# Optimization experiments

Measured on AMD Instinct MI355X. Metric: run time of the kernel, lower is better.

## Reference

```python
import math
import jax, jax.numpy as jnp
import numpy as np

N_EXPERTS = 8
CAPACITY_FACTOR = 1.25
AUX_COEF = 0.01  # forward passes aux_loss_coef to BOTH z-loss and lb-loss


def setup_inputs() -> dict:
    key = jax.random.key(0)
    k1, k2 = jax.random.split(key)
    B, T, D = 4, 4096, 2048
    x = jax.random.normal(k1, (B, T, D), dtype=jnp.float32)
    # nn.Linear(d_model, n_experts, bias=False) weight: (n_experts, d_model)
    W = jax.random.normal(k2, (N_EXPERTS, D), dtype=jnp.float32) * (1.0 / math.sqrt(D))
    return {"x": x, "W": W}


def reference(x, W):
    B, T, D = x.shape
    S = B * T
    E = W.shape[0]
    capacity = int(math.ceil(S / E * CAPACITY_FACTOR))  # static

    x_flat = x.reshape(S, D)
    logits = jnp.einsum("sd,ed->se", x_flat, W)          # (S, E)
    probs = jax.nn.softmax(logits, axis=-1)               # (S, E)
    gate_vals = jnp.max(probs, axis=-1)                   # (S,)
    expert_idx = jnp.argmax(probs, axis=-1)               # (S,) int

    # rank of each token within its expert's queue (token order), 0-based
    onehot = jax.nn.one_hot(expert_idx, E, dtype=jnp.int32)        # (S, E)
    rank = jnp.sum(jnp.cumsum(onehot, axis=0) * onehot, axis=-1) - 1  # (S,)
    keep = rank < capacity
    kept_gates = jnp.where(keep, gate_vals, jnp.zeros((), gate_vals.dtype))

    # z-loss: coef * mean(logsumexp(logits)^2)
    log_z = jax.scipy.special.logsumexp(logits, axis=-1)
    z_loss = AUX_COEF * jnp.mean(log_z * log_z)

    # load-balance loss: coef * E * sum(f_i * p_i)
    p = jnp.mean(probs, axis=0)                                     # (E,)
    counts = jnp.zeros((E,), dtype=probs.dtype).at[expert_idx].add(1.0)
    f = counts / S
    lb_loss = AUX_COEF * E * jnp.sum(f * p)

    aux_loss = z_loss + lb_loss
    return expert_idx, kept_gates, aux_loss
```

## Files before the change

kernel.cpp:

```cpp
#include <hip/hip_runtime.h>

#define S_TOKENS 16384
#define DMODEL   2048
#define NE       8
#define CAPACITY 2560
#define AUXC     0.01f


__global__ void init_kernel(float* __restrict__ acc) {
    int t = threadIdx.x;
    if (t < 9) acc[t] = 0.0f;
}

__global__ __launch_bounds__(512, 1) void logits_kernel(
    const float* __restrict__ x, const float* __restrict__ W,
    int* __restrict__ idx_out, float* __restrict__ gate_out,
    float* __restrict__ psum, float* __restrict__ zsum) {
    __shared__ float4 WA[DMODEL];
    __shared__ float4 WB[DMODEL];

    const int tid  = threadIdx.x;
    const int wave = tid >> 6;
    const int lane = tid & 63;

    for (int j = tid; j < DMODEL; j += 512) {
        WA[j] = make_float4(W[j],          W[DMODEL + j],   W[2*DMODEL + j], W[3*DMODEL + j]);
        WB[j] = make_float4(W[4*DMODEL+j], W[5*DMODEL + j], W[6*DMODEL + j], W[7*DMODEL + j]);
    }
    __syncthreads();

    float pacc = 0.0f;
    float zacc = 0.0f;

    for (int gi = 0; gi < 4; ++gi) {
        const int group = blockIdx.x * 4 + gi;
        const int token = group * 8 + wave;
        const float* __restrict__ xrow = x + (size_t)token * DMODEL;

        float a0=0,a1=0,a2=0,a3=0,a4=0,a5=0,a6=0,a7=0;
        #pragma unroll 8
        for (int k = 0; k < DMODEL/64; ++k) {
            float  xv = xrow[k*64 + lane];
            float4 wa = WA[k*64 + lane];
            float4 wb = WB[k*64 + lane];
            a0 += xv*wa.x; a1 += xv*wa.y; a2 += xv*wa.z; a3 += xv*wa.w;
            a4 += xv*wb.x; a5 += xv*wb.y; a6 += xv*wb.z; a7 += xv*wb.w;
        }
        #pragma unroll
        for (int off = 32; off > 0; off >>= 1) {
            a0 += __shfl_xor(a0, off); a1 += __shfl_xor(a1, off);
            a2 += __shfl_xor(a2, off); a3 += __shfl_xor(a3, off);
            a4 += __shfl_xor(a4, off); a5 += __shfl_xor(a5, off);
            a6 += __shfl_xor(a6, off); a7 += __shfl_xor(a7, off);
        }
        float m = a0; int e = 0;
        if (a1 > m) { m = a1; e = 1; }
        if (a2 > m) { m = a2; e = 2; }
        if (a3 > m) { m = a3; e = 3; }
        if (a4 > m) { m = a4; e = 4; }
        if (a5 > m) { m = a5; e = 5; }
        if (a6 > m) { m = a6; e = 6; }
        if (a7 > m) { m = a7; e = 7; }
        float z = expf(a0-m)+expf(a1-m)+expf(a2-m)+expf(a3-m)
                + expf(a4-m)+expf(a5-m)+expf(a6-m)+expf(a7-m);
        float gate = 1.0f / z;
        float lz   = m + logf(z);

        if (lane == 0) {
            idx_out[token]  = e;
            gate_out[token] = gate;
            zacc += lz * lz;
        }
        float ae = a0;
        if (lane == 1) ae = a1;
        if (lane == 2) ae = a2;
        if (lane == 3) ae = a3;
        if (lane == 4) ae = a4;
        if (lane == 5) ae = a5;
        if (lane == 6) ae = a6;
        if (lane == 7) ae = a7;
        if (lane < NE) pacc += expf(ae - m) * gate;
    }

    __syncthreads();
    float* red = (float*)WA;
    float* zrd = (float*)WB;
    if (lane < NE)  red[wave*8 + lane] = pacc;
    if (lane == 0)  zrd[wave] = zacc;
    __syncthreads();
    if (tid < NE) {
        float s = 0.0f;
        #pragma unroll
        for (int w = 0; w < 8; ++w) s += red[w*8 + tid];
        atomicAdd(&psum[tid], s);
    }
    if (tid == NE) {
        float s = 0.0f;
        #pragma unroll
        for (int w = 0; w < 8; ++w) s += zrd[w];
        atomicAdd(zsum, s);
    }
}

__global__ __launch_bounds__(256, 1) void scan_kernel(
    const int* __restrict__ idx, int* __restrict__ prefix,
    const float* __restrict__ psum, const float* __restrict__ zsum,
    float* __restrict__ aux_out) {
    __shared__ int arr[NE][256];
    const int t = threadIdx.x;

    unsigned clo = 0, chi = 0;
    const int base = t * 64;
    #pragma unroll 8
    for (int i = 0; i < 64; ++i) {
        int e = idx[base + i];
        if (e < 4) clo += 1u << (8*e);
        else       chi += 1u << (8*(e-4));
    }
    int cnt[8];
    cnt[0] = clo & 255; cnt[1] = (clo >> 8) & 255; cnt[2] = (clo >> 16) & 255; cnt[3] = clo >> 24;
    cnt[4] = chi & 255; cnt[5] = (chi >> 8) & 255; cnt[6] = (chi >> 16) & 255; cnt[7] = chi >> 24;
    #pragma unroll
    for (int e = 0; e < NE; ++e) arr[e][t] = cnt[e];
    __syncthreads();

    for (int off = 1; off < 256; off <<= 1) {
        int v[8];
        #pragma unroll
        for (int e = 0; e < NE; ++e) v[e] = (t >= off) ? arr[e][t - off] : 0;
        __syncthreads();
        #pragma unroll
        for (int e = 0; e < NE; ++e) arr[e][t] += v[e];
        __syncthreads();
    }
    #pragma unroll
    for (int e = 0; e < NE; ++e) prefix[t*8 + e] = arr[e][t] - cnt[e];

    if (t == 0) {
        float lb = 0.0f;
        for (int e = 0; e < NE; ++e) {
            float f = (float)arr[e][255] / (float)S_TOKENS;
            float p = psum[e] / (float)S_TOKENS;
            lb += f * p;
        }
        lb *= AUXC * (float)NE;
        float zl = AUXC * (zsum[0] / (float)S_TOKENS);
        aux_out[0] = zl + lb;
    }
}

__global__ __launch_bounds__(64, 1) void output_kernel(
    const int* __restrict__ idx, const float* __restrict__ gate,
    const int* __restrict__ prefix, float* __restrict__ out) {
    const int b = blockIdx.x;
    const int l = threadIdx.x;
    const int token = b*64 + l;
    const int e = idx[token];

    unsigned long long mymask = 0;
    #pragma unroll
    for (int q = 0; q < NE; ++q) {
        unsigned long long msk = __ballot(e == q);
        if (e == q) mymask = msk;
    }
    unsigned long long lt = (1ull << l) - 1ull;
    int rank = prefix[b*8 + e] + __popcll(mymask & lt);

    out[token] = (float)e;
    out[S_TOKENS + token] = (rank < CAPACITY) ? gate[token] : 0.0f;
}

extern "C" void kernel_launch(void* const* d_in, const int* in_sizes, int n_in,
                              void* d_out, int out_size, void* d_ws, size_t ws_size,
                              hipStream_t stream) {
    const float* x = (const float*)d_in[0];
    const float* W = (const float*)d_in[1];
    float* out = (float*)d_out;

    int*   ws_idx    = (int*)d_ws;
    float* ws_gate   = (float*)d_ws + 16384;
    int*   ws_prefix = (int*)d_ws + 32768;
    float* ws_psum   = (float*)d_ws + 34816;
    float* ws_zsum   = (float*)d_ws + 34824;

    init_kernel<<<1, 64, 0, stream>>>(ws_psum);
    logits_kernel<<<512, 512, 0, stream>>>(x, W, ws_idx, ws_gate, ws_psum, ws_zsum);
    scan_kernel<<<1, 256, 0, stream>>>(ws_idx, ws_prefix, ws_psum, ws_zsum, out + 2*S_TOKENS);
    output_kernel<<<256, 64, 0, stream>>>(ws_idx, ws_gate, ws_prefix, out);
}
```

Before: 209.5 us.

## Process four tokens per wave and fuse scan, loss and output into one kernel

The logits kernel now has each wave compute four tokens at once, reusing each shared-memory W load across four x rows. The four-way result is folded with a butterfly shuffle reduction that spreads the tokens across lane groups. Per-block partial sums are written to a workspace array instead of global atomics, which removes the init kernel. The scan, aux-loss and output kernels are merged into a single-block finalize kernel that counts per-expert tokens with ballots, scans them, and writes outputs. This saves launches, at the cost of running the output pass on a single block.

```diff
diff --git a/kernel.cpp b/kernel.cpp
--- a/kernel.cpp
+++ b/kernel.cpp
@@ -4,170 +4,201 @@
 #define DMODEL   2048
 #define NE       8
 #define CAPACITY 2560
-#define AUXC     0.01f
-
-
-__global__ void init_kernel(float* __restrict__ acc) {
-    int t = threadIdx.x;
-    if (t < 9) acc[t] = 0.0f;
-}
-
-__global__ __launch_bounds__(512, 1) void logits_kernel(
+
+
+__global__ __launch_bounds__(512, 4) void logits_kernel(
     const float* __restrict__ x, const float* __restrict__ W,
     int* __restrict__ idx_out, float* __restrict__ gate_out,
-    float* __restrict__ psum, float* __restrict__ zsum) {
+    float* __restrict__ partials) {
     __shared__ float4 WA[DMODEL];
     __shared__ float4 WB[DMODEL];
+    __shared__ float  sacc[16];
 
     const int tid  = threadIdx.x;
     const int wave = tid >> 6;
     const int lane = tid & 63;
 
+    if (tid < 16) sacc[tid] = 0.0f;
     for (int j = tid; j < DMODEL; j += 512) {
         WA[j] = make_float4(W[j],          W[DMODEL + j],   W[2*DMODEL + j], W[3*DMODEL + j]);
         WB[j] = make_float4(W[4*DMODEL+j], W[5*DMODEL + j], W[6*DMODEL + j], W[7*DMODEL + j]);
     }
     __syncthreads();
 
-    float pacc = 0.0f;
-    float zacc = 0.0f;
-
-    for (int gi = 0; gi < 4; ++gi) {
-        const int group = blockIdx.x * 4 + gi;
-        const int token = group * 8 + wave;
-        const float* __restrict__ xrow = x + (size_t)token * DMODEL;
-
-        float a0=0,a1=0,a2=0,a3=0,a4=0,a5=0,a6=0,a7=0;
-        #pragma unroll 8
-        for (int k = 0; k < DMODEL/64; ++k) {
-            float  xv = xrow[k*64 + lane];
-            float4 wa = WA[k*64 + lane];
-            float4 wb = WB[k*64 + lane];
-            a0 += xv*wa.x; a1 += xv*wa.y; a2 += xv*wa.z; a3 += xv*wa.w;
-            a4 += xv*wb.x; a5 += xv*wb.y; a6 += xv*wb.z; a7 += xv*wb.w;
-        }
-        #pragma unroll
-        for (int off = 32; off > 0; off >>= 1) {
-            a0 += __shfl_xor(a0, off); a1 += __shfl_xor(a1, off);
-            a2 += __shfl_xor(a2, off); a3 += __shfl_xor(a3, off);
-            a4 += __shfl_xor(a4, off); a5 += __shfl_xor(a5, off);
-            a6 += __shfl_xor(a6, off); a7 += __shfl_xor(a7, off);
-        }
-        float m = a0; int e = 0;
-        if (a1 > m) { m = a1; e = 1; }
-        if (a2 > m) { m = a2; e = 2; }
-        if (a3 > m) { m = a3; e = 3; }
-        if (a4 > m) { m = a4; e = 4; }
-        if (a5 > m) { m = a5; e = 5; }
-        if (a6 > m) { m = a6; e = 6; }
-        if (a7 > m) { m = a7; e = 7; }
-        float z = expf(a0-m)+expf(a1-m)+expf(a2-m)+expf(a3-m)
-                + expf(a4-m)+expf(a5-m)+expf(a6-m)+expf(a7-m);
-        float gate = 1.0f / z;
-        float lz   = m + logf(z);
-
-        if (lane == 0) {
-            idx_out[token]  = e;
-            gate_out[token] = gate;
-            zacc += lz * lz;
-        }
-        float ae = a0;
-        if (lane == 1) ae = a1;
-        if (lane == 2) ae = a2;
-        if (lane == 3) ae = a3;
-        if (lane == 4) ae = a4;
-        if (lane == 5) ae = a5;
-        if (lane == 6) ae = a6;
-        if (lane == 7) ae = a7;
-        if (lane < NE) pacc += expf(ae - m) * gate;
-    }
-
-    __syncthreads();
-    float* red = (float*)WA;
-    float* zrd = (float*)WB;
-    if (lane < NE)  red[wave*8 + lane] = pacc;
-    if (lane == 0)  zrd[wave] = zacc;
-    __syncthreads();
-    if (tid < NE) {
-        float s = 0.0f;
-        #pragma unroll
-        for (int w = 0; w < 8; ++w) s += red[w*8 + tid];
-        atomicAdd(&psum[tid], s);
-    }
-    if (tid == NE) {
-        float s = 0.0f;
-        #pragma unroll
-        for (int w = 0; w < 8; ++w) s += zrd[w];
-        atomicAdd(zsum, s);
-    }
+    const int token0 = blockIdx.x * 32 + wave * 4;
+    const float* __restrict__ x0 = x + (size_t)token0 * DMODEL;
+    const float* __restrict__ x1 = x0 + DMODEL;
+    const float* __restrict__ x2 = x1 + DMODEL;
+    const float* __restrict__ x3 = x2 + DMODEL;
+
+    float a0[NE], a1[NE], a2[NE], a3[NE];
+    #pragma unroll
+    for (int e = 0; e < NE; ++e) { a0[e]=0; a1[e]=0; a2[e]=0; a3[e]=0; }
+
+    #pragma unroll 4
+    for (int i = 0; i < DMODEL/64; ++i) {
+        const int j = i*64 + lane;
+        float xv0 = x0[j], xv1 = x1[j], xv2 = x2[j], xv3 = x3[j];
+        float4 wa = WA[j];
+        float4 wb = WB[j];
+        float wv[NE] = {wa.x, wa.y, wa.z, wa.w, wb.x, wb.y, wb.z, wb.w};
+        #pragma unroll
+        for (int e = 0; e < NE; ++e) {
+            float w = wv[e];
+            a0[e] += xv0*w; a1[e] += xv1*w; a2[e] += xv2*w; a3[e] += xv3*w;
+        }
+    }
+
+    const bool hiHalf = (lane & 32) != 0;
+    const bool oddQ   = (lane & 16) != 0;
+    float lg[NE];
+    #pragma unroll
+    for (int e = 0; e < NE; ++e) {
+        float s0 = a0[e] + __shfl_xor(a0[e], 32);
+        float s1 = a1[e] + __shfl_xor(a1[e], 32);
+        float s2 = a2[e] + __shfl_xor(a2[e], 32);
+        float s3 = a3[e] + __shfl_xor(a3[e], 32);
+        float u = hiHalf ? s2 : s0;
+        float v = hiHalf ? s3 : s1;
+        u += __shfl_xor(u, 16);
+        v += __shfl_xor(v, 16);
+        float r = oddQ ? v : u;
+        r += __shfl_xor(r, 8);
+        r += __shfl_xor(r, 4);
+        r += __shfl_xor(r, 2);
+        r += __shfl_xor(r, 1);
+        lg[e] = r;
+    }
+
+    const int token = token0 + (lane >> 4);
+    const int sub   = lane & 15;
+
+    float m = lg[0]; int e = 0;
+    #pragma unroll
+    for (int k = 1; k < NE; ++k) { if (lg[k] > m) { m = lg[k]; e = k; } }
+    float z = 0.0f;
+    #pragma unroll
+    for (int k = 0; k < NE; ++k) z += expf(lg[k] - m);
+    float gate = 1.0f / z;
+    float lz   = m + logf(z);
+
+    if (sub == 0) {
+        idx_out[token]  = e;
+        gate_out[token] = gate;
+        atomicAdd(&sacc[8], lz * lz);
+    }
+    if (sub < NE) {
+        float b0 = (sub & 1) ? lg[1] : lg[0];
+        float b1 = (sub & 1) ? lg[3] : lg[2];
+        float b2 = (sub & 1) ? lg[5] : lg[4];
+        float b3 = (sub & 1) ? lg[7] : lg[6];
+        float c0 = (sub & 2) ? b1 : b0;
+        float c1 = (sub & 2) ? b3 : b2;
+        float ae = (sub & 4) ? c1 : c0;
+        atomicAdd(&sacc[sub], expf(ae - m) * gate);
+    }
+
+    __syncthreads();
+    if (tid < 9) partials[tid*512 + blockIdx.x] = sacc[tid];
 }
 
-__global__ __launch_bounds__(256, 1) void scan_kernel(
-    const int* __restrict__ idx, int* __restrict__ prefix,
-    const float* __restrict__ psum, const float* __restrict__ zsum,
-    float* __restrict__ aux_out) {
-    __shared__ int arr[NE][256];
-    const int t = threadIdx.x;
-
-    unsigned clo = 0, chi = 0;
-    const int base = t * 64;
-    #pragma unroll 8
-    for (int i = 0; i < 64; ++i) {
-        int e = idx[base + i];
-        if (e < 4) clo += 1u << (8*e);
-        else       chi += 1u << (8*(e-4));
-    }
-    int cnt[8];
-    cnt[0] = clo & 255; cnt[1] = (clo >> 8) & 255; cnt[2] = (clo >> 16) & 255; cnt[3] = clo >> 24;
-    cnt[4] = chi & 255; cnt[5] = (chi >> 8) & 255; cnt[6] = (chi >> 16) & 255; cnt[7] = chi >> 24;
-    #pragma unroll
-    for (int e = 0; e < NE; ++e) arr[e][t] = cnt[e];
-    __syncthreads();
-
+__global__ __launch_bounds__(512, 1) void finalize_kernel(
+    const int* __restrict__ idx, const float* __restrict__ gate,
+    const float* __restrict__ partials, float* __restrict__ out) {
+    __shared__ float facc[9];
+    __shared__ int   cnt[256][9];
+    const int t    = threadIdx.x;
+    const int wv   = t >> 6;
+    const int lane = t & 63;
+
+    if (t < 9) facc[t] = 0.0f;
+    __syncthreads();
+
+    {
+        float v = partials[0*512 + t];
+        #pragma unroll
+        for (int off = 32; off > 0; off >>= 1) v += __shfl_xor(v, off);
+        if (lane == 0) atomicAdd(&facc[0], v);
+    }
+    #pragma unroll
+    for (int q = 1; q < 9; ++q) {
+        float v = partials[q*512 + t];
+        #pragma unroll
+        for (int off = 32; off > 0; off >>= 1) v += __shfl_xor(v, off);
+        if (lane == 0) atomicAdd(&facc[q], v);
+    }
+
+    const int spanBeg = wv * 32, spanEnd = spanBeg + 32;
+    {
+        int e = idx[spanBeg*64 + lane];
+        for (int s = spanBeg; s < spanEnd; ++s) {
+            int en = (s+1 < spanEnd) ? idx[(s+1)*64 + lane] : 0;
+            #pragma unroll
+            for (int q = 0; q < NE; ++q) {
+                unsigned long long mk = __ballot(e == q);
+                if (lane == q) cnt[s][q] = (int)__popcll(mk);
+            }
+            e = en;
+        }
+    }
+    __syncthreads();
+
+    int myc[NE];
+    if (t < 256) {
+        #pragma unroll
+        for (int q = 0; q < NE; ++q) myc[q] = cnt[t][q];
+    }
     for (int off = 1; off < 256; off <<= 1) {
-        int v[8];
-        #pragma unroll
-        for (int e = 0; e < NE; ++e) v[e] = (t >= off) ? arr[e][t - off] : 0;
+        int v[NE];
+        if (t < 256) {
+            #pragma unroll
+            for (int q = 0; q < NE; ++q) v[q] = (t >= off) ? cnt[t-off][q] : 0;
+        }
         __syncthreads();
-        #pragma unroll
-        for (int e = 0; e < NE; ++e) arr[e][t] += v[e];
+        if (t < 256) {
+            #pragma unroll
+            for (int q = 0; q < NE; ++q) cnt[t][q] += v[q];
+        }
         __syncthreads();
     }
-    #pragma unroll
-    for (int e = 0; e < NE; ++e) prefix[t*8 + e] = arr[e][t] - cnt[e];
 
     if (t == 0) {
         float lb = 0.0f;
-        for (int e = 0; e < NE; ++e) {
-            float f = (float)arr[e][255] / (float)S_TOKENS;
-            float p = psum[e] / (float)S_TOKENS;
+        #pragma unroll
+        for (int q = 0; q < NE; ++q) {
+            float f = (float)cnt[255][q] * (1.0f/S_TOKENS);
+            float p = facc[q] * (1.0f/S_TOKENS);
             lb += f * p;
         }
-        lb *= AUXC * (float)NE;
-        float zl = AUXC * (zsum[0] / (float)S_TOKENS);
-        aux_out[0] = zl + lb;
-    }
-}
-
-__global__ __launch_bounds__(64, 1) void output_kernel(
-    const int* __restrict__ idx, const float* __restrict__ gate,
-    const int* __restrict__ prefix, float* __restrict__ out) {
-    const int b = blockIdx.x;
-    const int l = threadIdx.x;
-    const int token = b*64 + l;
-    const int e = idx[token];
-
-    unsigned long long mymask = 0;
-    #pragma unroll
-    for (int q = 0; q < NE; ++q) {
-        unsigned long long msk = __ballot(e == q);
-        if (e == q) mymask = msk;
-    }
-    unsigned long long lt = (1ull << l) - 1ull;
-    int rank = prefix[b*8 + e] + __popcll(mymask & lt);
-
-    out[token] = (float)e;
-    out[S_TOKENS + token] = (rank < CAPACITY) ? gate[token] : 0.0f;
+        out[2*S_TOKENS] = 0.01f * (facc[8] * (1.0f/S_TOKENS)) + 0.08f * lb;
+    }
+    __syncthreads();
+    if (t < 256) {
+        #pragma unroll
+        for (int q = 0; q < NE; ++q) cnt[t][q] -= myc[q];
+    }
+    __syncthreads();
+
+    {
+        int   e = idx[spanBeg*64 + lane];
+        float g = gate[spanBeg*64 + lane];
+        for (int s = spanBeg; s < spanEnd; ++s) {
+            int   en = (s+1 < spanEnd) ? idx[(s+1)*64 + lane]  : 0;
+            float gn = (s+1 < spanEnd) ? gate[(s+1)*64 + lane] : 0.0f;
+            unsigned long long mym = 0;
+            #pragma unroll
+            for (int q = 0; q < NE; ++q) {
+                unsigned long long mk = __ballot(e == q);
+                if (e == q) mym = mk;
+            }
+            unsigned long long lt = (1ull << lane) - 1ull;
+            int rank = cnt[s][e] + (int)__popcll(mym & lt);
+            int token = s*64 + lane;
+            out[token] = (float)e;
+            out[S_TOKENS + token] = (rank < CAPACITY) ? g : 0.0f;
+            e = en; g = gn;
+        }
+    }
 }
 
 extern "C" void kernel_launch(void* const* d_in, const int* in_sizes, int n_in,
@@ -177,14 +208,10 @@
     const float* W = (const float*)d_in[1];
     float* out = (float*)d_out;
 
-    int*   ws_idx    = (int*)d_ws;
-    float* ws_gate   = (float*)d_ws + 16384;
-    int*   ws_prefix = (int*)d_ws + 32768;
-    float* ws_psum   = (float*)d_ws + 34816;
-    float* ws_zsum   = (float*)d_ws + 34824;
-
-    init_kernel<<<1, 64, 0, stream>>>(ws_psum);
-    logits_kernel<<<512, 512, 0, stream>>>(x, W, ws_idx, ws_gate, ws_psum, ws_zsum);
-    scan_kernel<<<1, 256, 0, stream>>>(ws_idx, ws_prefix, ws_psum, ws_zsum, out + 2*S_TOKENS);
-    output_kernel<<<256, 64, 0, stream>>>(ws_idx, ws_gate, ws_prefix, out);
+    int*   ws_idx  = (int*)d_ws;
+    float* ws_gate = (float*)d_ws + 16384;
+    float* ws_part = (float*)d_ws + 32768;
+
+    logits_kernel<<<512, 512, 0, stream>>>(x, W, ws_idx, ws_gate, ws_part);
+    finalize_kernel<<<1, 512, 0, stream>>>(ws_idx, ws_gate, ws_part, out);
 }
```

New measurement: 234.8 us. 12.1% more time.
